# Performance work log

Hardware: AMD Instinct MI355X
Metric: run time of the kernel (lower is better)

Reference implementation:

```python
import jax, jax.numpy as jnp
import numpy as np

B, N, D, H, DK, MS, FF = 8, 256, 256, 16, 16, 16, 512
EPS = 1e-5


def _inorm(x, scale, bias):
    # InstanceNorm1d over the node dim (axis=1) per channel, affine
    m = jnp.mean(x, axis=1, keepdims=True)
    v = jnp.var(x, axis=1, keepdims=True)
    return (x - m) * jax.lax.rsqrt(v + EPS) * scale + bias


def _heads(x):
    b, n, _ = x.shape
    return x.reshape(b, n, H, DK).transpose(0, 2, 1, 3)  # (b,H,n,DK)


def _block(emb_r, emb_c, cost, Wq, Wk, Wv, m1w, m1b, m2w, m2b, cw, cb,
           n1s, n1b, w1, b1, w2, b2, n2s, n2b):
    b, n, _ = emb_r.shape
    q = _heads(emb_r @ Wq)
    k = _heads(emb_c @ Wk)
    v = _heads(emb_c @ Wv)
    dot = jnp.einsum('bhid,bhjd->bhij', q, k) / jnp.sqrt(jnp.float32(DK))
    # stack dot-product score with cost-matrix score: (b,H,r,c,2)
    two = jnp.stack([dot, jnp.broadcast_to(cost[:, None], dot.shape)], axis=-1)
    # per-head 2 -> MS -> 1 MLP on each (row,col) score pair
    ms1 = jax.nn.relu(jnp.einsum('bhrcs,hsm->bhrcm', two, m1w)
                      + m1b[None, :, None, None, :])
    mixed = jnp.einsum('bhrcm,hm->bhrc', ms1, m2w[:, :, 0]) \
            + m2b[:, 0][None, :, None, None]
    w = jax.nn.softmax(mixed, axis=-1)
    out = jnp.einsum('bhrc,bhcd->bhrd', w, v)
    out_concat = out.transpose(0, 2, 1, 3).reshape(b, n, H * DK)
    mh = out_concat @ cw + cb
    out1 = _inorm(emb_r + mh, n1s, n1b)
    ff = jax.nn.relu(out1 @ w1 + b1) @ w2 + b2
    return _inorm(out1 + ff, n2s, n2b)


def setup_inputs() -> dict:
    key = jax.random.key(0)
    keys = iter(jax.random.split(key, 64))
    def nrm(shape, s=0.05):
        return jax.random.normal(next(keys), shape, dtype=jnp.float32) * s
    inp = {
        'row_emb': nrm((B, N, D), 1.0),
        'col_emb': nrm((B, N, D), 1.0),
        'cost_mat': jax.random.uniform(next(keys), (B, N, N), dtype=jnp.float32),
    }
    for p in ('r', 'c'):
        inp[p + 'Wq'] = nrm((D, H * DK)); inp[p + 'Wk'] = nrm((D, H * DK)); inp[p + 'Wv'] = nrm((D, H * DK))
        inp[p + 'm1w'] = nrm((H, 2, MS), 0.5); inp[p + 'm1b'] = nrm((H, MS), 0.5)
        inp[p + 'm2w'] = nrm((H, MS, 1), 0.25); inp[p + 'm2b'] = nrm((H, 1), 0.25)
        inp[p + 'cw'] = nrm((H * DK, D)); inp[p + 'cb'] = jnp.zeros((D,), jnp.float32)
        inp[p + 'n1s'] = jnp.ones((D,), jnp.float32); inp[p + 'n1b'] = jnp.zeros((D,), jnp.float32)
        inp[p + 'w1'] = nrm((D, FF)); inp[p + 'b1'] = jnp.zeros((FF,), jnp.float32)
        inp[p + 'w2'] = nrm((FF, D)); inp[p + 'b2'] = jnp.zeros((D,), jnp.float32)
        inp[p + 'n2s'] = jnp.ones((D,), jnp.float32); inp[p + 'n2b'] = jnp.zeros((D,), jnp.float32)
    return inp


def reference(row_emb, col_emb, cost_mat,
              rWq, rWk, rWv, rm1w, rm1b, rm2w, rm2b, rcw, rcb,
              rn1s, rn1b, rw1, rb1, rw2, rb2, rn2s, rn2b,
              cWq, cWk, cWv, cm1w, cm1b, cm2w, cm2b, ccw, ccb,
              cn1s, cn1b, cw1, cb1, cw2, cb2, cn2s, cn2b):
    row_out = _block(row_emb, col_emb, cost_mat,
                     rWq, rWk, rWv, rm1w, rm1b, rm2w, rm2b, rcw, rcb,
                     rn1s, rn1b, rw1, rb1, rw2, rb2, rn2s, rn2b)
    col_out = _block(col_emb, row_emb, cost_mat.transpose(0, 2, 1),
                     cWq, cWk, cWv, cm1w, cm1b, cm2w, cm2b, ccw, ccb,
                     cn1s, cn1b, cw1, cb1, cw2, cb2, cn2s, cn2b)
    return row_out, col_out
```

## Files before the change

kernel.cpp:

```cpp
#include <hip/hip_runtime.h>
#include <hip/hip_bf16.h>
#include <hip/hip_fp16.h>

#define Bc 8
#define Nc 256
#define Dc 256
#define Hc 16
#define DKc 16
#define MSc 16
#define FFc 512
#define SZc 524288
#define WHALF 524288
#define FFH 1048576

typedef __hip_bfloat16 bf16;
typedef __attribute__((ext_vector_type(8))) short bfrag8;
typedef __attribute__((ext_vector_type(4))) float f32x4;

__device__ __forceinline__ short f2bs(float x) {
    bf16 t = __float2bfloat16(x);
    return *reinterpret_cast<short*>(&t);
}

__device__ __forceinline__ __half2 pk_relu(__half2 x) {
    __half2 r;
    asm("v_pk_max_f16 %0, %1, 0" : "=v"(r) : "v"(x));
    return r;
}

__global__ void setup_kernel(const float* __restrict__ e0, const float* __restrict__ e1,
                             bf16* __restrict__ o0, bf16* __restrict__ o1,
                             float* __restrict__ statsB,
                             const float* rWq, const float* rWk, const float* rWv,
                             const float* rcw, const float* rw1, const float* rw2,
                             const float* cWq, const float* cWk, const float* cWv,
                             const float* ccw, const float* cw1, const float* cw2,
                             const float* rm1w, const float* rm1b, const float* rm2w,
                             const float* cm1w, const float* cm1b, const float* cm2w,
                             __half2* __restrict__ Wpk,
                             bf16* __restrict__ WT) {
    int y = blockIdx.y;
    if (y < 2) {
        const float* src = y ? e1 : e0;
        bf16* dst = y ? o1 : o0;
        size_t base = (size_t)blockIdx.x * 2048 + threadIdx.x;
#pragma unroll
        for (int i = 0; i < 8; ++i)
            dst[base + i * 256] = __float2bfloat16(src[base + i * 256]);
        return;
    }
    if (y == 2) {
        if (blockIdx.x < 64) {
            statsB[blockIdx.x * 256 + threadIdx.x] = 0.f;
        } else if (blockIdx.x < 66) {
            int p = blockIdx.x - 64;
            const float* m1w = p ? cm1w : rm1w;
            const float* m1b = p ? cm1b : rm1b;
            const float* m2w = p ? cm2w : rm2w;
            int h = threadIdx.x >> 4, m = threadIdx.x & 15;
            __half2* wp = Wpk + (size_t)(p * 16 + h) * 64;
            wp[m]      = __float2half2_rn(m1w[h * 32 + m] * 0.25f);
            wp[16 + m] = __float2half2_rn(m1w[h * 32 + 16 + m]);
            wp[32 + m] = __float2half2_rn(m1b[h * 16 + m]);
            wp[48 + m] = __float2half2_rn(m2w[h * 16 + m]);
        }
        return;
    }
    int z = y - 3;
    int p = z / 6, widx = z % 6;
    const float* src; int K, N; size_t off;
    switch (widx) {
        case 0: src = p ? cWq : rWq; K = 256; N = 256; off = 0; break;
        case 1: src = p ? cWk : rWk; K = 256; N = 256; off = 65536; break;
        case 2: src = p ? cWv : rWv; K = 256; N = 256; off = 131072; break;
        case 3: src = p ? ccw : rcw; K = 256; N = 256; off = 196608; break;
        case 4: src = p ? cw1 : rw1; K = 256; N = 512; off = 262144; break;
        default: src = p ? cw2 : rw2; K = 512; N = 256; off = 393216; break;
    }
    int Ntiles = N >> 5, Ktiles = K >> 5;
    if ((int)blockIdx.x >= Ktiles * Ntiles) return;
    int kt = blockIdx.x / Ntiles, nt = blockIdx.x - kt * Ntiles;
    int k0 = kt * 32, n0 = nt * 32;
    bf16* dst = WT + (size_t)p * WHALF + off;
    __shared__ float t[32][33];
    int tx = threadIdx.x & 31, ty = threadIdx.x >> 5;
#pragma unroll
    for (int i = 0; i < 4; ++i)
        t[ty + i * 8][tx] = src[(size_t)(k0 + ty + i * 8) * N + n0 + tx];
    __syncthreads();
#pragma unroll
    for (int i = 0; i < 4; ++i)
        dst[(size_t)(n0 + ty + i * 8) * K + k0 + tx] = __float2bfloat16(t[tx][ty + i * 8]);
}

__global__ void gemm_qkv_kernel(const short* __restrict__ embRb, const short* __restrict__ embCb,
                                const short* __restrict__ WT, bf16* __restrict__ qkv) {
    int z = blockIdx.z;
    int p = z / 3, j = z % 3;
    const short* A  = (j == 0) ? (p ? embCb : embRb) : (p ? embRb : embCb);
    const short* BT = WT + (size_t)p * WHALF + j * 65536;
    bf16* out = qkv + (size_t)z * SZc;

    int lane = threadIdx.x & 63, w = threadIdx.x >> 6;
    int m_base = blockIdx.x * 64 + (w & 1) * 32;
    int n_base = blockIdx.y * 64 + (w >> 1) * 32;
    int mr = lane & 15, quad = lane >> 4;

    const short* pa0 = A + (size_t)(m_base + mr) * 256 + quad * 8;
    const short* pa1 = pa0 + 16 * 256;
    const short* pb0 = BT + (size_t)(n_base + mr) * 256 + quad * 8;
    const short* pb1 = pb0 + 16 * 256;

    f32x4 acc00 = {0.f, 0.f, 0.f, 0.f}, acc01 = {0.f, 0.f, 0.f, 0.f};
    f32x4 acc10 = {0.f, 0.f, 0.f, 0.f}, acc11 = {0.f, 0.f, 0.f, 0.f};
#pragma unroll
    for (int kt = 0; kt < 256; kt += 32) {
        bfrag8 A0 = *(const bfrag8*)(pa0 + kt);
        bfrag8 A1 = *(const bfrag8*)(pa1 + kt);
        bfrag8 B0 = *(const bfrag8*)(pb0 + kt);
        bfrag8 B1 = *(const bfrag8*)(pb1 + kt);
        acc00 = __builtin_amdgcn_mfma_f32_16x16x32_bf16(A0, B0, acc00, 0, 0, 0);
        acc01 = __builtin_amdgcn_mfma_f32_16x16x32_bf16(A0, B1, acc01, 0, 0, 0);
        acc10 = __builtin_amdgcn_mfma_f32_16x16x32_bf16(A1, B0, acc10, 0, 0, 0);
        acc11 = __builtin_amdgcn_mfma_f32_16x16x32_bf16(A1, B1, acc11, 0, 0, 0);
    }

#pragma unroll
    for (int jt = 0; jt < 2; ++jt) {
        int col = n_base + jt * 16 + mr;
        int h = col >> 4, dk = col & 15;
        f32x4 a0 = jt ? acc01 : acc00;
        f32x4 a1 = jt ? acc11 : acc10;
#pragma unroll
        for (int r = 0; r < 4; ++r) {
            int row0 = m_base + quad * 4 + r;
            int row1 = row0 + 16;
            int b0 = row0 >> 8, n0 = row0 & 255;
            int b1 = row1 >> 8, n1 = row1 & 255;
            out[((size_t)(b0 * Hc + h) * Nc + n0) * DKc + dk] = __float2bfloat16(a0[r]);
            out[((size_t)(b1 * Hc + h) * Nc + n1) * DKc + dk] = __float2bfloat16(a1[r]);
        }
    }
}

__global__ void attn_kernel(const short* __restrict__ qkv, const float* __restrict__ cost,
                            const __half2* __restrict__ Wpk,
                            const float* rm2b, const float* cm2b,
                            bf16* __restrict__ attnb) {
    int b = blockIdx.x, h = blockIdx.y;
    int p = blockIdx.z >> 4, rc = blockIdx.z & 15;
    const short* Q = qkv + (size_t)(p * 3 + 0) * SZc;
    const short* K = qkv + (size_t)(p * 3 + 1) * SZc;
    const short* V = qkv + (size_t)(p * 3 + 2) * SZc;
    const __half2* wp = Wpk + (size_t)(p * 16 + h) * 64;
    float b2v = (p ? cm2b : rm2b)[h];
    bf16* out_concat = attnb + (size_t)p * SZc;

    int bh = b * Hc + h;
    int r0 = rc * 16;
    int c = threadIdx.x;
    int lane = c & 63, wid = c >> 6;
    int mr = lane & 15, quad = lane >> 4;

    __shared__ __align__(16) short sVT[16 * 264];
    __shared__ __align__(16) short sEb[16 * 264];
    __shared__ float sPart[4 * 256];
    __shared__ float sSum[16 * 4];

    {
        const short* vp = V + ((size_t)bh * Nc + c) * DKc;
        bfrag8 v0 = *(const bfrag8*)vp;
        bfrag8 v1 = *(const bfrag8*)(vp + 8);
#pragma unroll
        for (int i = 0; i < 8; ++i) {
            sVT[i * 264 + c]       = v0[i];
            sVT[(8 + i) * 264 + c] = v1[i];
        }
    }

    bfrag8 qf = {0, 0, 0, 0, 0, 0, 0, 0};
    if (quad < 2)
        qf = *(const bfrag8*)(Q + ((size_t)bh * Nc + r0 + mr) * DKc + quad * 8);

    __half2 sv2[8];
#pragma unroll
    for (int t = 0; t < 4; ++t) {
        bfrag8 kf = {0, 0, 0, 0, 0, 0, 0, 0};
        if (quad < 2)
            kf = *(const bfrag8*)(K + ((size_t)bh * Nc + wid * 64 + t * 16 + mr) * DKc + quad * 8);
        f32x4 acc = {0.f, 0.f, 0.f, 0.f};
        acc = __builtin_amdgcn_mfma_f32_16x16x32_bf16(qf, kf, acc, 0, 0, 0);
        sv2[t * 2]     = __floats2half2_rn(acc[0], acc[1]);
        sv2[t * 2 + 1] = __floats2half2_rn(acc[2], acc[3]);
    }

    const float* costR = cost + (size_t)b * Nc * Nc;
    __half2 cv2[8];
    if (p) {
#pragma unroll
        for (int t = 0; t < 4; ++t) {
            float4 cvv = *(const float4*)(costR +
                (size_t)(wid * 64 + t * 16 + mr) * Nc + r0 + quad * 4);
            cv2[t * 2]     = __floats2half2_rn(cvv.x, cvv.y);
            cv2[t * 2 + 1] = __floats2half2_rn(cvv.z, cvv.w);
        }
    } else {
#pragma unroll
        for (int t = 0; t < 4; ++t) {
            float c0 = costR[(size_t)(r0 + quad * 4 + 0) * Nc + wid * 64 + t * 16 + mr];
            float c1 = costR[(size_t)(r0 + quad * 4 + 1) * Nc + wid * 64 + t * 16 + mr];
            float c2 = costR[(size_t)(r0 + quad * 4 + 2) * Nc + wid * 64 + t * 16 + mr];
            float c3 = costR[(size_t)(r0 + quad * 4 + 3) * Nc + wid * 64 + t * 16 + mr];
            cv2[t * 2]     = __floats2half2_rn(c0, c1);
            cv2[t * 2 + 1] = __floats2half2_rn(c2, c3);
        }
    }

    __syncthreads();

    const __half2 z2 = __half2half2(__float2half(0.f));
    __half2 mix2[8] = {z2, z2, z2, z2, z2, z2, z2, z2};
#pragma unroll
    for (int m = 0; m < MSc; ++m) {
        __half2 w1d = wp[m];
        __half2 w1c = wp[16 + m];
        __half2 b1v = wp[32 + m];
        __half2 w2v = wp[48 + m];
#pragma unroll
        for (int s = 0; s < 8; ++s) {
            __half2 tt = __hfma2(sv2[s], w1d, __hfma2(cv2[s], w1c, b1v));
            mix2[s] = __hfma2(pk_relu(tt), w2v, mix2[s]);
        }
    }
    float ex[16];
#pragma unroll
    for (int s = 0; s < 8; ++s) {
        float2 mf = __half22float2(mix2[s]);
        ex[s * 2]     = __expf(mf.x + b2v);
        ex[s * 2 + 1] = __expf(mf.y + b2v);
    }

#pragma unroll
    for (int t = 0; t < 4; ++t)
#pragma unroll
        for (int r = 0; r < 4; ++r)
            sEb[(quad * 4 + r) * 264 + wid * 64 + t * 16 + mr] = f2bs(ex[t * 4 + r]);

#pragma unroll
    for (int r = 0; r < 4; ++r) {
        float rp = ex[r] + ex[4 + r] + ex[8 + r] + ex[12 + r];
        rp += __shfl_xor(rp, 1);
        rp += __shfl_xor(rp, 2);
        rp += __shfl_xor(rp, 4);
        rp += __shfl_xor(rp, 8);
        if (mr == 0) sSum[(quad * 4 + r) * 4 + wid] = rp;
    }
    __syncthreads();

    {
        const short* pa = &sEb[mr * 264 + wid * 64 + quad * 8];
        const short* pb = &sVT[mr * 264 + wid * 64 + quad * 8];
        f32x4 acc = {0.f, 0.f, 0.f, 0.f};
        bfrag8 a0 = *(const bfrag8*)pa;
        bfrag8 b0 = *(const bfrag8*)pb;
        acc = __builtin_amdgcn_mfma_f32_16x16x32_bf16(a0, b0, acc, 0, 0, 0);
        bfrag8 a1 = *(const bfrag8*)(pa + 32);
        bfrag8 b1 = *(const bfrag8*)(pb + 32);
        acc = __builtin_amdgcn_mfma_f32_16x16x32_bf16(a1, b1, acc, 0, 0, 0);
#pragma unroll
        for (int r = 0; r < 4; ++r)
            sPart[wid * 256 + (quad * 4 + r) * 16 + mr] = acc[r];
    }
    __syncthreads();

    {
        int r = c >> 4, dk = c & 15;
        float o = sPart[c] + sPart[256 + c] + sPart[512 + c] + sPart[768 + c];
        float sum = sSum[r * 4] + sSum[r * 4 + 1] + sSum[r * 4 + 2] + sSum[r * 4 + 3];
        out_concat[((size_t)(b * Nc + r0 + r)) * Dc + h * DKc + dk] =
            __float2bfloat16(o / sum);
    }
}

__global__ void gemm_cat_kernel(const short* __restrict__ attnb, const short* __restrict__ WT,
                                const float* rcb, const float* ccb,
                                const float* __restrict__ resR, const float* __restrict__ resC,
                                float* __restrict__ x1, float* __restrict__ stats1) {
    int p = blockIdx.z;
    const short* A  = attnb + (size_t)p * SZc;
    const short* BT = WT + (size_t)p * WHALF + 196608;
    const float* bias = p ? ccb : rcb;
    const float* res  = p ? resC : resR;
    float* outF = x1 + (size_t)p * SZc;
    float* st   = stats1 + p * 4096;

    int lane = threadIdx.x & 63, w = threadIdx.x >> 6;
    int m_base = blockIdx.x * 64 + (w & 1) * 32;
    int n_base = blockIdx.y * 64 + (w >> 1) * 32;
    int mr = lane & 15, quad = lane >> 4;

    const short* pa0 = A + (size_t)(m_base + mr) * 256 + quad * 8;
    const short* pa1 = pa0 + (size_t)16 * 256;
    const short* pb0 = BT + (size_t)(n_base + mr) * 256 + quad * 8;
    const short* pb1 = pb0 + (size_t)16 * 256;

    f32x4 acc00 = {0.f, 0.f, 0.f, 0.f}, acc01 = {0.f, 0.f, 0.f, 0.f};
    f32x4 acc10 = {0.f, 0.f, 0.f, 0.f}, acc11 = {0.f, 0.f, 0.f, 0.f};
#pragma unroll
    for (int kt = 0; kt < 256; kt += 32) {
        bfrag8 A0 = *(const bfrag8*)(pa0 + kt);
        bfrag8 A1 = *(const bfrag8*)(pa1 + kt);
        bfrag8 B0 = *(const bfrag8*)(pb0 + kt);
        bfrag8 B1 = *(const bfrag8*)(pb1 + kt);
        acc00 = __builtin_amdgcn_mfma_f32_16x16x32_bf16(A0, B0, acc00, 0, 0, 0);
        acc01 = __builtin_amdgcn_mfma_f32_16x16x32_bf16(A0, B1, acc01, 0, 0, 0);
        acc10 = __builtin_amdgcn_mfma_f32_16x16x32_bf16(A1, B0, acc10, 0, 0, 0);
        acc11 = __builtin_amdgcn_mfma_f32_16x16x32_bf16(A1, B1, acc11, 0, 0, 0);
    }

    int bb = m_base >> 8;
#pragma unroll
    for (int jt = 0; jt < 2; ++jt) {
        int col = n_base + jt * 16 + mr;
        float bv = bias[col];
        f32x4 a0 = jt ? acc01 : acc00;
        f32x4 a1 = jt ? acc11 : acc10;
        float ssum = 0.f, ssq = 0.f;
#pragma unroll
        for (int r = 0; r < 4; ++r) {
            int row0 = m_base + quad * 4 + r;
            int row1 = row0 + 16;
            float v0 = a0[r] + bv + res[(size_t)row0 * 256 + col];
            float v1 = a1[r] + bv + res[(size_t)row1 * 256 + col];
            outF[(size_t)row0 * 256 + col] = v0;
            outF[(size_t)row1 * 256 + col] = v1;
            ssum += v0 + v1;
            ssq  += v0 * v0 + v1 * v1;
        }
        atomicAdd(&st[(bb * 256 + col) * 2],     ssum);
        atomicAdd(&st[(bb * 256 + col) * 2 + 1], ssq);
    }
}

__global__ __launch_bounds__(256) void gemm_ff1n_kernel(
        const float* __restrict__ x1, const float* __restrict__ stats1,
        const float* rn1s, const float* rn1b, const float* cn1s, const float* cn1b,
        const short* __restrict__ WT, const float* rb1, const float* cb1,
        bf16* __restrict__ ffh) {
    int p = blockIdx.z;
    const float* X   = x1 + (size_t)p * SZc;
    const float* st  = stats1 + p * 4096;
    const float* n1s = p ? cn1s : rn1s;
    const float* n1b = p ? cn1b : rn1b;
    const short* BT  = WT + (size_t)p * WHALF + 262144;
    const float* bias = p ? cb1 : rb1;
    bf16* outB = ffh + (size_t)p * FFH;

    __shared__ __align__(16) short sA[64 * 264];
    int c = threadIdx.x;
    int m_base = blockIdx.x * 64;
    int b = m_base >> 8;

    float s = st[(b * 256 + c) * 2];
    float q = st[(b * 256 + c) * 2 + 1];
    float mean = s * (1.f / Nc);
    float var = q * (1.f / Nc) - mean * mean;
    float inv = rsqrtf(var + 1e-5f) * n1s[c];
    float nb = n1b[c];
#pragma unroll 8
    for (int i = 0; i < 64; ++i) {
        float v = X[(size_t)(m_base + i) * 256 + c];
        sA[i * 264 + c] = f2bs((v - mean) * inv + nb);
    }
    __syncthreads();

    int lane = c & 63, w = c >> 6;
    int mloc = (w & 1) * 32;
    int n_base = blockIdx.y * 64 + (w >> 1) * 32;
    int mr = lane & 15, quad = lane >> 4;

    const short* pa0 = &sA[(mloc + mr) * 264 + quad * 8];
    const short* pa1 = pa0 + 16 * 264;
    const short* pb0 = BT + (size_t)(n_base + mr) * 256 + quad * 8;
    const short* pb1 = pb0 + 16 * 256;

    f32x4 acc00 = {0.f, 0.f, 0.f, 0.f}, acc01 = {0.f, 0.f, 0.f, 0.f};
    f32x4 acc10 = {0.f, 0.f, 0.f, 0.f}, acc11 = {0.f, 0.f, 0.f, 0.f};
#pragma unroll
    for (int kt = 0; kt < 256; kt += 32) {
        bfrag8 A0 = *(const bfrag8*)(pa0 + kt);
        bfrag8 A1 = *(const bfrag8*)(pa1 + kt);
        bfrag8 B0 = *(const bfrag8*)(pb0 + kt);
        bfrag8 B1 = *(const bfrag8*)(pb1 + kt);
        acc00 = __builtin_amdgcn_mfma_f32_16x16x32_bf16(A0, B0, acc00, 0, 0, 0);
        acc01 = __builtin_amdgcn_mfma_f32_16x16x32_bf16(A0, B1, acc01, 0, 0, 0);
        acc10 = __builtin_amdgcn_mfma_f32_16x16x32_bf16(A1, B0, acc10, 0, 0, 0);
        acc11 = __builtin_amdgcn_mfma_f32_16x16x32_bf16(A1, B1, acc11, 0, 0, 0);
    }

#pragma unroll
    for (int jt = 0; jt < 2; ++jt) {
        int col = n_base + jt * 16 + mr;
        float bv = bias[col];
        f32x4 a0 = jt ? acc01 : acc00;
        f32x4 a1 = jt ? acc11 : acc10;
#pragma unroll
        for (int r = 0; r < 4; ++r) {
            int row0 = m_base + mloc + quad * 4 + r;
            int row1 = row0 + 16;
            outB[(size_t)row0 * 512 + col] = __float2bfloat16(fmaxf(a0[r] + bv, 0.f));
            outB[(size_t)row1 * 512 + col] = __float2bfloat16(fmaxf(a1[r] + bv, 0.f));
        }
    }
}

__global__ void gemm_ff2n_kernel(const short* __restrict__ ffh, const short* __restrict__ WT,
                                 const float* rb2, const float* cb2,
                                 const float* __restrict__ x1, const float* __restrict__ stats1,
                                 const float* rn1s, const float* rn1b,
                                 const float* cn1s, const float* cn1b,
                                 float* __restrict__ ff2, float* __restrict__ stats2) {
    int p = blockIdx.z;
    const short* A  = ffh + (size_t)p * FFH;
    const short* BT = WT + (size_t)p * WHALF + 393216;
    const float* bias = p ? cb2 : rb2;
    const float* X   = x1 + (size_t)p * SZc;
    const float* st1 = stats1 + p * 4096;
    const float* n1s = p ? cn1s : rn1s;
    const float* n1b = p ? cn1b : rn1b;
    float* outF = ff2 + (size_t)p * SZc;
    float* st2  = stats2 + p * 4096;

    int lane = threadIdx.x & 63, w = threadIdx.x >> 6;
    int m_base = blockIdx.x * 64 + (w & 1) * 32;
    int n_base = blockIdx.y * 64 + (w >> 1) * 32;
    int mr = lane & 15, quad = lane >> 4;

    const short* pa0 = A + (size_t)(m_base + mr) * 512 + quad * 8;
    const short* pa1 = pa0 + (size_t)16 * 512;
    const short* pb0 = BT + (size_t)(n_base + mr) * 512 + quad * 8;
    const short* pb1 = pb0 + (size_t)16 * 512;

    f32x4 acc00 = {0.f, 0.f, 0.f, 0.f}, acc01 = {0.f, 0.f, 0.f, 0.f};
    f32x4 acc10 = {0.f, 0.f, 0.f, 0.f}, acc11 = {0.f, 0.f, 0.f, 0.f};
#pragma unroll
    for (int kt = 0; kt < 512; kt += 32) {
        bfrag8 A0 = *(const bfrag8*)(pa0 + kt);
        bfrag8 A1 = *(const bfrag8*)(pa1 + kt);
        bfrag8 B0 = *(const bfrag8*)(pb0 + kt);
        bfrag8 B1 = *(const bfrag8*)(pb1 + kt);
        acc00 = __builtin_amdgcn_mfma_f32_16x16x32_bf16(A0, B0, acc00, 0, 0, 0);
        acc01 = __builtin_amdgcn_mfma_f32_16x16x32_bf16(A0, B1, acc01, 0, 0, 0);
        acc10 = __builtin_amdgcn_mfma_f32_16x16x32_bf16(A1, B0, acc10, 0, 0, 0);
        acc11 = __builtin_amdgcn_mfma_f32_16x16x32_bf16(A1, B1, acc11, 0, 0, 0);
    }

    int bb = m_base >> 8;
#pragma unroll
    for (int jt = 0; jt < 2; ++jt) {
        int col = n_base + jt * 16 + mr;
        float s1 = st1[(bb * 256 + col) * 2];
        float q1 = st1[(bb * 256 + col) * 2 + 1];
        float mean1 = s1 * (1.f / Nc);
        float var1 = q1 * (1.f / Nc) - mean1 * mean1;
        float inv1 = rsqrtf(var1 + 1e-5f) * n1s[col];
        float nb1 = n1b[col];
        float bv = bias[col];
        f32x4 a0 = jt ? acc01 : acc00;
        f32x4 a1 = jt ? acc11 : acc10;
        float ssum = 0.f, ssq = 0.f;
#pragma unroll
        for (int r = 0; r < 4; ++r) {
            int row0 = m_base + quad * 4 + r;
            int row1 = row0 + 16;
            float res0 = (X[(size_t)row0 * 256 + col] - mean1) * inv1 + nb1;
            float res1 = (X[(size_t)row1 * 256 + col] - mean1) * inv1 + nb1;
            float v0 = a0[r] + bv + res0;
            float v1 = a1[r] + bv + res1;
            outF[(size_t)row0 * 256 + col] = v0;
            outF[(size_t)row1 * 256 + col] = v1;
            ssum += v0 + v1;
            ssq  += v0 * v0 + v1 * v1;
        }
        atomicAdd(&st2[(bb * 256 + col) * 2],     ssum);
        atomicAdd(&st2[(bb * 256 + col) * 2 + 1], ssq);
    }
}

__global__ void apply_kernel(const float* __restrict__ x, const float* __restrict__ stats,
                             const float* sR, const float* bR,
                             const float* sC, const float* bC,
                             float* __restrict__ outF) {
    int p = blockIdx.y;
    int t = threadIdx.x;
    int row = blockIdx.x * 4 + (t >> 6);
    int d0 = (t & 63) * 4;
    int b = row >> 8;
    const float* st = stats + p * 4096 + (size_t)(b * 256 + d0) * 2;
    float4 s01 = *(const float4*)st;
    float4 s23 = *(const float4*)(st + 4);
    const float* sp = p ? sC : sR;
    const float* bp = p ? bC : bR;
    float4 sc = *(const float4*)(sp + d0);
    float4 bi = *(const float4*)(bp + d0);
    float4 v = *(const float4*)(x + (size_t)p * SZc + (size_t)row * Dc + d0);
    float sums[4] = {s01.x, s01.z, s23.x, s23.z};
    float sqs[4]  = {s01.y, s01.w, s23.y, s23.w};
    float vv[4]   = {v.x, v.y, v.z, v.w};
    float scs[4]  = {sc.x, sc.y, sc.z, sc.w};
    float bis[4]  = {bi.x, bi.y, bi.z, bi.w};
    float4 o;
#pragma unroll
    for (int j = 0; j < 4; ++j) {
        float mean = sums[j] * (1.f / Nc);
        float var = sqs[j] * (1.f / Nc) - mean * mean;
        float inv = rsqrtf(var + 1e-5f);
        ((float*)&o)[j] = (vv[j] - mean) * inv * scs[j] + bis[j];
    }
    *(float4*)(outF + (size_t)p * SZc + (size_t)row * Dc + d0) = o;
}

extern "C" void kernel_launch(void* const* d_in, const int* in_sizes, int n_in,
                              void* d_out, int out_size, void* d_ws, size_t ws_size,
                              hipStream_t stream) {
    const float* row_emb = (const float*)d_in[0];
    const float* col_emb = (const float*)d_in[1];
    const float* cost    = (const float*)d_in[2];
    float* out = (float*)d_out;
    float* ws = (float*)d_ws;
#define RP(i) ((const float*)d_in[3 + (i)])
#define CP(i) ((const float*)d_in[20 + (i)])

    float* x1     = ws;
    float* ff2    = ws + 2 * (size_t)SZc;
    float* statsB = ws + 4 * (size_t)SZc;
    __half2* Wpk  = (__half2*)(statsB + 16384);
    bf16* bfbase  = (bf16*)(Wpk + 4096);
    bf16* qkvb  = bfbase;
    bf16* embRb = qkvb + 6 * (size_t)SZc;
    bf16* embCb = embRb + SZc;
    bf16* attnb = embCb + SZc;
    bf16* ffh   = attnb + 2 * (size_t)SZc;
    bf16* WT    = ffh + 4 * (size_t)SZc;
    float* stats1 = statsB;
    float* stats2 = statsB + 8192;

    setup_kernel<<<dim3(256, 15), 256, 0, stream>>>(
        row_emb, col_emb, embRb, embCb, statsB,
        RP(0), RP(1), RP(2), RP(7), RP(11), RP(13),
        CP(0), CP(1), CP(2), CP(7), CP(11), CP(13),
        RP(3), RP(4), RP(5), CP(3), CP(4), CP(5), Wpk, WT);
    gemm_qkv_kernel<<<dim3(32, 4, 6), 256, 0, stream>>>(
        (const short*)embRb, (const short*)embCb, (const short*)WT, qkvb);
    attn_kernel<<<dim3(Bc, Hc, 32), 256, 0, stream>>>(
        (const short*)qkvb, cost, Wpk, RP(6), CP(6), attnb);
    gemm_cat_kernel<<<dim3(32, 4, 2), 256, 0, stream>>>(
        (const short*)attnb, (const short*)WT, RP(8), CP(8), row_emb, col_emb, x1, stats1);
    gemm_ff1n_kernel<<<dim3(32, 8, 2), 256, 0, stream>>>(
        x1, stats1, RP(9), RP(10), CP(9), CP(10),
        (const short*)WT, RP(12), CP(12), ffh);
    gemm_ff2n_kernel<<<dim3(32, 4, 2), 256, 0, stream>>>(
        (const short*)ffh, (const short*)WT, RP(14), CP(14),
        x1, stats1, RP(9), RP(10), CP(9), CP(10), ff2, stats2);
    apply_kernel<<<dim3(512, 2), 256, 0, stream>>>(
        ff2, stats2, RP(15), RP(16), CP(15), CP(16), out);
#undef RP
#undef CP
}
```

Before: 203.3 us.

## Precompute fp16 cost and transposed cost, loop four row tiles per attention block

The setup kernel now converts the cost matrix to fp16 once, in both natural and transposed layouts, so attention reads half-width contiguous 8-byte values instead of strided fp32 loads for the row-block path. Each attention block now handles 64 rows in a loop of four 16-row tiles. This reuses the V-transpose staging and the K fragments across tiles and cuts the grid by four. In exchange there are extra workspace buffers, additional setup work, an extra barrier per tile, and fewer blocks to hide latency.

```diff
diff --git a/kernel.cpp b/kernel.cpp
--- a/kernel.cpp
+++ b/kernel.cpp
@@ -22,6 +22,11 @@
     return *reinterpret_cast<short*>(&t);
 }
 
+__device__ __forceinline__ short f2hs(float x) {
+    __half t = __float2half(x);
+    return *reinterpret_cast<short*>(&t);
+}
+
 __device__ __forceinline__ __half2 pk_relu(__half2 x) {
     __half2 r;
     asm("v_pk_max_f16 %0, %1, 0" : "=v"(r) : "v"(x));
@@ -31,6 +36,8 @@
 __global__ void setup_kernel(const float* __restrict__ e0, const float* __restrict__ e1,
                              bf16* __restrict__ o0, bf16* __restrict__ o1,
                              float* __restrict__ statsB,
+                             const float* __restrict__ cost,
+                             short* __restrict__ costH, short* __restrict__ costHT,
                              const float* rWq, const float* rWk, const float* rWv,
                              const float* rcw, const float* rw1, const float* rw2,
                              const float* cWq, const float* cWk, const float* cWv,
@@ -66,6 +73,30 @@
         }
         return;
     }
+    if (y == 15) {
+        size_t base = (size_t)blockIdx.x * 2048 + threadIdx.x;
+#pragma unroll
+        for (int i = 0; i < 8; ++i)
+            costH[base + i * 256] = f2hs(cost[base + i * 256]);
+        return;
+    }
+    __shared__ float t[32][33];
+    int tx = threadIdx.x & 31, ty = threadIdx.x >> 5;
+    if (y >= 16) {
+        int tl = blockIdx.x + (y - 16) * 256;
+        int bb = tl >> 6, t2 = tl & 63;
+        int r0 = (t2 >> 3) * 32, c0 = (t2 & 7) * 32;
+        const float* src = cost + (size_t)bb * 65536;
+        short* dst = costHT + (size_t)bb * 65536;
+#pragma unroll
+        for (int i = 0; i < 4; ++i)
+            t[ty + i * 8][tx] = src[(size_t)(r0 + ty + i * 8) * 256 + c0 + tx];
+        __syncthreads();
+#pragma unroll
+        for (int i = 0; i < 4; ++i)
+            dst[(size_t)(c0 + ty + i * 8) * 256 + r0 + tx] = f2hs(t[tx][ty + i * 8]);
+        return;
+    }
     int z = y - 3;
     int p = z / 6, widx = z % 6;
     const float* src; int K, N; size_t off;
@@ -82,8 +113,6 @@
     int kt = blockIdx.x / Ntiles, nt = blockIdx.x - kt * Ntiles;
     int k0 = kt * 32, n0 = nt * 32;
     bf16* dst = WT + (size_t)p * WHALF + off;
-    __shared__ float t[32][33];
-    int tx = threadIdx.x & 31, ty = threadIdx.x >> 5;
 #pragma unroll
     for (int i = 0; i < 4; ++i)
         t[ty + i * 8][tx] = src[(size_t)(k0 + ty + i * 8) * N + n0 + tx];
@@ -143,12 +172,14 @@
     }
 }
 
-__global__ void attn_kernel(const short* __restrict__ qkv, const float* __restrict__ cost,
+__global__ void attn_kernel(const short* __restrict__ qkv,
+                            const short* __restrict__ costH,
+                            const short* __restrict__ costHT,
                             const __half2* __restrict__ Wpk,
                             const float* rm2b, const float* cm2b,
                             bf16* __restrict__ attnb) {
     int b = blockIdx.x, h = blockIdx.y;
-    int p = blockIdx.z >> 4, rc = blockIdx.z & 15;
+    int p = blockIdx.z >> 2, rcg = blockIdx.z & 3;
     const short* Q = qkv + (size_t)(p * 3 + 0) * SZc;
     const short* K = qkv + (size_t)(p * 3 + 1) * SZc;
     const short* V = qkv + (size_t)(p * 3 + 2) * SZc;
@@ -157,7 +188,7 @@
     bf16* out_concat = attnb + (size_t)p * SZc;
 
     int bh = b * Hc + h;
-    int r0 = rc * 16;
+    int r0base = rcg * 64;
     int c = threadIdx.x;
     int lane = c & 63, wid = c >> 6;
     int mr = lane & 15, quad = lane >> 4;
@@ -178,107 +209,108 @@
         }
     }
 
-    bfrag8 qf = {0, 0, 0, 0, 0, 0, 0, 0};
-    if (quad < 2)
-        qf = *(const bfrag8*)(Q + ((size_t)bh * Nc + r0 + mr) * DKc + quad * 8);
-
-    __half2 sv2[8];
+    bfrag8 kf[4];
 #pragma unroll
     for (int t = 0; t < 4; ++t) {
-        bfrag8 kf = {0, 0, 0, 0, 0, 0, 0, 0};
+        bfrag8 z = {0, 0, 0, 0, 0, 0, 0, 0};
+        kf[t] = z;
         if (quad < 2)
-            kf = *(const bfrag8*)(K + ((size_t)bh * Nc + wid * 64 + t * 16 + mr) * DKc + quad * 8);
-        f32x4 acc = {0.f, 0.f, 0.f, 0.f};
-        acc = __builtin_amdgcn_mfma_f32_16x16x32_bf16(qf, kf, acc, 0, 0, 0);
-        sv2[t * 2]     = __floats2half2_rn(acc[0], acc[1]);
-        sv2[t * 2 + 1] = __floats2half2_rn(acc[2], acc[3]);
-    }
-
-    const float* costR = cost + (size_t)b * Nc * Nc;
-    __half2 cv2[8];
-    if (p) {
+            kf[t] = *(const bfrag8*)(K + ((size_t)bh * Nc + wid * 64 + t * 16 + mr) * DKc + quad * 8);
+    }
+
+    const __half2* cp = (const __half2*)((p ? costH : costHT) + (size_t)b * 65536);
+
+    __syncthreads();
+
+    for (int tile = 0; tile < 4; ++tile) {
+        int r0 = r0base + tile * 16;
+
+        bfrag8 qf = {0, 0, 0, 0, 0, 0, 0, 0};
+        if (quad < 2)
+            qf = *(const bfrag8*)(Q + ((size_t)bh * Nc + r0 + mr) * DKc + quad * 8);
+
+        __half2 sv2[8];
 #pragma unroll
         for (int t = 0; t < 4; ++t) {
-            float4 cvv = *(const float4*)(costR +
-                (size_t)(wid * 64 + t * 16 + mr) * Nc + r0 + quad * 4);
-            cv2[t * 2]     = __floats2half2_rn(cvv.x, cvv.y);
-            cv2[t * 2 + 1] = __floats2half2_rn(cvv.z, cvv.w);
-        }
-    } else {
+            f32x4 acc = {0.f, 0.f, 0.f, 0.f};
+            acc = __builtin_amdgcn_mfma_f32_16x16x32_bf16(qf, kf[t], acc, 0, 0, 0);
+            sv2[t * 2]     = __floats2half2_rn(acc[0], acc[1]);
+            sv2[t * 2 + 1] = __floats2half2_rn(acc[2], acc[3]);
+        }
+
+        __half2 cv2[8];
 #pragma unroll
         for (int t = 0; t < 4; ++t) {
-            float c0 = costR[(size_t)(r0 + quad * 4 + 0) * Nc + wid * 64 + t * 16 + mr];
-            float c1 = costR[(size_t)(r0 + quad * 4 + 1) * Nc + wid * 64 + t * 16 + mr];
-            float c2 = costR[(size_t)(r0 + quad * 4 + 2) * Nc + wid * 64 + t * 16 + mr];
-            float c3 = costR[(size_t)(r0 + quad * 4 + 3) * Nc + wid * 64 + t * 16 + mr];
-            cv2[t * 2]     = __floats2half2_rn(c0, c1);
-            cv2[t * 2 + 1] = __floats2half2_rn(c2, c3);
-        }
-    }
-
-    __syncthreads();
-
-    const __half2 z2 = __half2half2(__float2half(0.f));
-    __half2 mix2[8] = {z2, z2, z2, z2, z2, z2, z2, z2};
-#pragma unroll
-    for (int m = 0; m < MSc; ++m) {
-        __half2 w1d = wp[m];
-        __half2 w1c = wp[16 + m];
-        __half2 b1v = wp[32 + m];
-        __half2 w2v = wp[48 + m];
+            int col = wid * 64 + t * 16 + mr;
+            int h2i = (col << 7) + (r0 >> 1) + (quad << 1);
+            uint2 u = *(const uint2*)(cp + h2i);
+            cv2[t * 2]     = *reinterpret_cast<__half2*>(&u.x);
+            cv2[t * 2 + 1] = *reinterpret_cast<__half2*>(&u.y);
+        }
+
+        const __half2 z2 = __half2half2(__float2half(0.f));
+        __half2 mix2[8] = {z2, z2, z2, z2, z2, z2, z2, z2};
+#pragma unroll
+        for (int m = 0; m < MSc; ++m) {
+            __half2 w1d = wp[m];
+            __half2 w1c = wp[16 + m];
+            __half2 b1v = wp[32 + m];
+            __half2 w2v = wp[48 + m];
+#pragma unroll
+            for (int s = 0; s < 8; ++s) {
+                __half2 tt = __hfma2(sv2[s], w1d, __hfma2(cv2[s], w1c, b1v));
+                mix2[s] = __hfma2(pk_relu(tt), w2v, mix2[s]);
+            }
+        }
+        float ex[16];
 #pragma unroll
         for (int s = 0; s < 8; ++s) {
-            __half2 tt = __hfma2(sv2[s], w1d, __hfma2(cv2[s], w1c, b1v));
-            mix2[s] = __hfma2(pk_relu(tt), w2v, mix2[s]);
-        }
-    }
-    float ex[16];
-#pragma unroll
-    for (int s = 0; s < 8; ++s) {
-        float2 mf = __half22float2(mix2[s]);
-        ex[s * 2]     = __expf(mf.x + b2v);
-        ex[s * 2 + 1] = __expf(mf.y + b2v);
-    }
-
-#pragma unroll
-    for (int t = 0; t < 4; ++t)
-#pragma unroll
-        for (int r = 0; r < 4; ++r)
-            sEb[(quad * 4 + r) * 264 + wid * 64 + t * 16 + mr] = f2bs(ex[t * 4 + r]);
-
-#pragma unroll
-    for (int r = 0; r < 4; ++r) {
-        float rp = ex[r] + ex[4 + r] + ex[8 + r] + ex[12 + r];
-        rp += __shfl_xor(rp, 1);
-        rp += __shfl_xor(rp, 2);
-        rp += __shfl_xor(rp, 4);
-        rp += __shfl_xor(rp, 8);
-        if (mr == 0) sSum[(quad * 4 + r) * 4 + wid] = rp;
-    }
-    __syncthreads();
-
-    {
-        const short* pa = &sEb[mr * 264 + wid * 64 + quad * 8];
-        const short* pb = &sVT[mr * 264 + wid * 64 + quad * 8];
-        f32x4 acc = {0.f, 0.f, 0.f, 0.f};
-        bfrag8 a0 = *(const bfrag8*)pa;
-        bfrag8 b0 = *(const bfrag8*)pb;
-        acc = __builtin_amdgcn_mfma_f32_16x16x32_bf16(a0, b0, acc, 0, 0, 0);
-        bfrag8 a1 = *(const bfrag8*)(pa + 32);
-        bfrag8 b1 = *(const bfrag8*)(pb + 32);
-        acc = __builtin_amdgcn_mfma_f32_16x16x32_bf16(a1, b1, acc, 0, 0, 0);
-#pragma unroll
-        for (int r = 0; r < 4; ++r)
-            sPart[wid * 256 + (quad * 4 + r) * 16 + mr] = acc[r];
-    }
-    __syncthreads();
-
-    {
-        int r = c >> 4, dk = c & 15;
-        float o = sPart[c] + sPart[256 + c] + sPart[512 + c] + sPart[768 + c];
-        float sum = sSum[r * 4] + sSum[r * 4 + 1] + sSum[r * 4 + 2] + sSum[r * 4 + 3];
-        out_concat[((size_t)(b * Nc + r0 + r)) * Dc + h * DKc + dk] =
-            __float2bfloat16(o / sum);
+            float2 mf = __half22float2(mix2[s]);
+            ex[s * 2]     = __expf(mf.x + b2v);
+            ex[s * 2 + 1] = __expf(mf.y + b2v);
+        }
+
+#pragma unroll
+        for (int t = 0; t < 4; ++t)
+#pragma unroll
+            for (int r = 0; r < 4; ++r)
+                sEb[(quad * 4 + r) * 264 + wid * 64 + t * 16 + mr] = f2bs(ex[t * 4 + r]);
+
+#pragma unroll
+        for (int r = 0; r < 4; ++r) {
+            float rp = ex[r] + ex[4 + r] + ex[8 + r] + ex[12 + r];
+            rp += __shfl_xor(rp, 1);
+            rp += __shfl_xor(rp, 2);
+            rp += __shfl_xor(rp, 4);
+            rp += __shfl_xor(rp, 8);
+            if (mr == 0) sSum[(quad * 4 + r) * 4 + wid] = rp;
+        }
+        __syncthreads();
+
+        {
+            const short* pa = &sEb[mr * 264 + wid * 64 + quad * 8];
+            const short* pb = &sVT[mr * 264 + wid * 64 + quad * 8];
+            f32x4 acc = {0.f, 0.f, 0.f, 0.f};
+            bfrag8 a0 = *(const bfrag8*)pa;
+            bfrag8 b0 = *(const bfrag8*)pb;
+            acc = __builtin_amdgcn_mfma_f32_16x16x32_bf16(a0, b0, acc, 0, 0, 0);
+            bfrag8 a1 = *(const bfrag8*)(pa + 32);
+            bfrag8 b1 = *(const bfrag8*)(pb + 32);
+            acc = __builtin_amdgcn_mfma_f32_16x16x32_bf16(a1, b1, acc, 0, 0, 0);
+#pragma unroll
+            for (int r = 0; r < 4; ++r)
+                sPart[wid * 256 + (quad * 4 + r) * 16 + mr] = acc[r];
+        }
+        __syncthreads();
+
+        {
+            int r = c >> 4, dk = c & 15;
+            float o = sPart[c] + sPart[256 + c] + sPart[512 + c] + sPart[768 + c];
+            float sum = sSum[r * 4] + sSum[r * 4 + 1] + sSum[r * 4 + 2] + sSum[r * 4 + 3];
+            out_concat[((size_t)(b * Nc + r0 + r)) * Dc + h * DKc + dk] =
+                __float2bfloat16(o / sum);
+        }
+        __syncthreads();
     }
 }
 
@@ -542,18 +574,21 @@
     bf16* attnb = embCb + SZc;
     bf16* ffh   = attnb + 2 * (size_t)SZc;
     bf16* WT    = ffh + 4 * (size_t)SZc;
+    short* costH  = (short*)(WT + 2 * (size_t)WHALF);
+    short* costHT = costH + SZc;
     float* stats1 = statsB;
     float* stats2 = statsB + 8192;
 
-    setup_kernel<<<dim3(256, 15), 256, 0, stream>>>(
+    setup_kernel<<<dim3(256, 18), 256, 0, stream>>>(
         row_emb, col_emb, embRb, embCb, statsB,
+        cost, costH, costHT,
         RP(0), RP(1), RP(2), RP(7), RP(11), RP(13),
         CP(0), CP(1), CP(2), CP(7), CP(11), CP(13),
         RP(3), RP(4), RP(5), CP(3), CP(4), CP(5), Wpk, WT);
     gemm_qkv_kernel<<<dim3(32, 4, 6), 256, 0, stream>>>(
         (const short*)embRb, (const short*)embCb, (const short*)WT, qkvb);
-    attn_kernel<<<dim3(Bc, Hc, 32), 256, 0, stream>>>(
-        (const short*)qkvb, cost, Wpk, RP(6), CP(6), attnb);
+    attn_kernel<<<dim3(Bc, Hc, 8), 256, 0, stream>>>(
+        (const short*)qkvb, costH, costHT, Wpk, RP(6), CP(6), attnb);
     gemm_cat_kernel<<<dim3(32, 4, 2), 256, 0, stream>>>(
         (const short*)attnb, (const short*)WT, RP(8), CP(8), row_emb, col_emb, x1, stats1);
     gemm_ff1n_kernel<<<dim3(32, 8, 2), 256, 0, stream>>>(
```

Result: no change. 206.9 us (+1.7%).
